# Kernel tuning notes

Measured on AMD Instinct MI355X. Metric: run time of the kernel, lower is better.

## Reference

```python
import jax, jax.numpy as jnp
import numpy as np

EPS = 1e-15
MAX_TANH_ARG = 1.0 - 1e-5  # clamp for artanh domain, standard in Poincare-ball libs


def logmap0(x):
    # Poincare ball, c=1: logmap0(x) = artanh(||x||) * x / ||x||
    norm = jnp.linalg.norm(x, axis=-1, keepdims=True)
    norm_c = jnp.clip(norm, EPS, MAX_TANH_ARG)
    scale = jnp.arctanh(norm_c) / jnp.maximum(norm, EPS)
    return scale * x


def expmap0(v):
    # Poincare ball, c=1: expmap0(v) = tanh(||v||) * v / ||v||
    norm = jnp.linalg.norm(v, axis=-1, keepdims=True)
    scale = jnp.tanh(norm) / jnp.maximum(norm, EPS)
    return scale * v


def setup_inputs() -> dict:
    key = jax.random.key(0)
    k1, k2, k3, k4 = jax.random.split(key, 4)
    N, E, D_IN, D_OUT = 50000, 600000, 128, 128
    # points loosely inside/near the ball; logmap0 clamps the norm anyway
    x = jax.random.uniform(k1, (N, D_IN), dtype=jnp.float32)
    edge_index = jax.random.randint(k2, (2, E), 0, N, dtype=jnp.int32)
    W = jax.random.normal(k3, (D_OUT, D_IN), dtype=jnp.float32) / np.sqrt(D_IN)
    b = jax.random.normal(k4, (D_OUT,), dtype=jnp.float32) * 0.01
    return {"x": x, "edge_index": edge_index, "W": W, "b": b}


def reference(x, edge_index, W, b):
    num_nodes = x.shape[0]
    src, dst = edge_index[0], edge_index[1]

    x_tangent = logmap0(x)                       # [N, D_in]
    h = x_tangent @ W.T + b                      # [N, D_out]

    # symmetric degree count: each edge adds 1 to dst and 1 to src
    ones = jnp.ones(src.shape[0], dtype=jnp.float32)
    deg = (jax.ops.segment_sum(ones, dst, num_segments=num_nodes)
           + jax.ops.segment_sum(ones, src, num_segments=num_nodes))
    deg = jnp.maximum(deg, 1.0)
    dinv = deg ** -0.5                           # [N]

    # fused gather-scale-scatter across ALL feature dims at once
    msg = h[src] * (dinv[src] * dinv[dst])[:, None]   # [E, D_out]
    out = jax.ops.segment_sum(msg, dst, num_segments=num_nodes)  # [N, D_out]

    return expmap0(out)
```

## Files before the change

### kernel.cpp

```cpp
#include <hip/hip_runtime.h>
#include <math.h>

#define D 128
#define CAP 48
#define NS 64
#define HB2 (NS * 2)
#define HBT (HB2 * 2)
#define HLDS 28672
#define BKB 128

typedef __attribute__((ext_vector_type(8))) short short8;
typedef __attribute__((ext_vector_type(4))) float f32x4;

__device__ inline unsigned short f2bf(float f) {
  unsigned int u = __float_as_uint(f);
  u = (u + 0x7FFFu + ((u >> 16) & 1u)) >> 16;
  return (unsigned short)u;
}
__device__ inline float bf2f(unsigned int us) {
  return __uint_as_float(us << 16);
}

__global__ __launch_bounds__(256) void k_prep(
    const float* __restrict__ W, const int* __restrict__ src,
    const int* __restrict__ dst, unsigned short* __restrict__ Wbf,
    unsigned int* __restrict__ cursor, unsigned char* __restrict__ part8,
    unsigned char* __restrict__ rank, int N, int E, int HP, int fancy) {
  const int t = threadIdx.x;
  const int bid = blockIdx.x;

  if (bid < HBT) {
    if (!fancy) return;
    __shared__ unsigned int lh[HLDS / 4];
    const int kind = bid >> 7;
    const int sb = bid & 127;
    const int s = sb >> 1, hf = sb & 1;
    const int H = (N + 1) >> 1;
    const int G16 = (H + 15) >> 4;
    for (int i = t; i < G16; i += 256) ((uint4*)lh)[i] = make_uint4(0, 0, 0, 0);
    __syncthreads();
    const int e0 = (int)((long long)s * E / NS);
    const int e1 = (int)((long long)(s + 1) * E / NS);
    const int hbase = hf * H;
    if (kind == 0) {
      for (int e = e0 + t; e < e1; e += 256) {
        int n = dst[e];
        unsigned int lw = (unsigned)(n - hbase);
        if (lw < (unsigned)H) {
          int sh = (lw & 3) << 3;
          unsigned int old = atomicAdd(&lh[lw >> 2], 1u << sh);
          rank[e] = (unsigned char)((old >> sh) & 0xFFu);
        }
      }
    } else {
      for (int e = e0 + t; e < e1; e += 256) {
        int n = src[e];
        unsigned int lw = (unsigned)(n - hbase);
        if (lw < (unsigned)H) atomicAdd(&lh[lw >> 2], 1u << ((lw & 3) << 3));
      }
    }
    __syncthreads();
    uint4* po = (uint4*)(part8 + (size_t)bid * HP);
    for (int i = t; i < G16; i += 256) po[i] = ((const uint4*)lh)[i];
    return;
  }

  int g = (bid - HBT) * 256 + t;
  if (g < N) cursor[g] = 0u;
  int i = g * 4;
  if (i < D * D) {
    float4 wv = *(const float4*)(W + i);
    int r = i >> 7, c = i & 127;
    int idx = ((c >> 3) << 10) + (r << 3) + (c & 7);
    *(ushort4*)(&Wbf[idx]) =
        make_ushort4(f2bf(wv.x), f2bf(wv.y), f2bf(wv.z), f2bf(wv.w));
  }
}

__global__ __launch_bounds__(256) void k_reduce(
    const unsigned char* __restrict__ part8, float* __restrict__ dinv,
    unsigned int* __restrict__ cntv, unsigned short* __restrict__ pre, int N,
    int HP) {
  int n = blockIdx.x * 256 + threadIdx.x;
  if (n >= N) return;
  const int H = (N + 1) >> 1;
  int hf = (n >= H);
  int lw = n - hf * H;
  unsigned int run = 0, so = 0;
  unsigned int pk[NS / 2];
#pragma unroll
  for (int s = 0; s < NS; ++s) {
    unsigned int cin = part8[(size_t)(s * 2 + hf) * HP + lw];
    unsigned int cot = part8[(size_t)(HB2 + s * 2 + hf) * HP + lw];
    if (s & 1)
      pk[s >> 1] |= run << 16;
    else
      pk[s >> 1] = run;
    run += cin;
    so += cot;
  }
  uint4* pp = (uint4*)(pre + (size_t)n * NS);
#pragma unroll
  for (int i = 0; i < NS / 8; ++i)
    pp[i] = make_uint4(pk[i * 4], pk[i * 4 + 1], pk[i * 4 + 2], pk[i * 4 + 3]);
  cntv[n] = run;
  dinv[n] = rsqrtf(fmaxf((float)(run + so), 1.0f));
}

__global__ __launch_bounds__(256) void k_main(
    const float* __restrict__ x, const unsigned short* __restrict__ Wbf,
    const float* __restrict__ bvec, const int* __restrict__ src,
    const int* __restrict__ dst, unsigned int* __restrict__ cursor,
    int* __restrict__ ebuf, const unsigned char* __restrict__ rank,
    const unsigned short* __restrict__ pre, unsigned short* __restrict__ h,
    int N, int E, int fancy) {
  const int t = threadIdx.x;
  const int bid = blockIdx.x;

  if (bid < BKB) {
    if (fancy) {
      const int s = bid >> 1;
      const int e0 = (int)((long long)s * E / NS);
      const int e1 = (int)((long long)(s + 1) * E / NS);
      for (int e = e0 + (bid & 1) * 256 + t; e < e1; e += 512) {
        int d_ = dst[e];
        unsigned int slot =
            (unsigned int)pre[(size_t)d_ * NS + s] + (unsigned int)rank[e];
        if (slot < CAP) ebuf[(size_t)d_ * CAP + slot] = src[e];
      }
    } else {
      const int e0 = (int)((long long)bid * E / BKB);
      const int e1 = (int)((long long)(bid + 1) * E / BKB);
      for (int e = e0 + t; e < e1; e += 256) {
        int d_ = dst[e], s_ = src[e];
        unsigned int p = atomicAdd(&cursor[d_], 1u) & 0xFFFFu;
        if (p < CAP) ebuf[(size_t)d_ * CAP + p] = s_;
        atomicAdd(&cursor[s_], 0x10000u);
      }
    }
    return;
  }

  const int gb = bid - BKB;
  const int w = t >> 6;
  const int l = t & 63;
  const int lc = l & 15;
  const int q = l >> 4;
  const int r0 = gb * 64;
  const int grow = r0 + w * 16 + lc;
  const bool ok = grow < N;
  const float* xp = x + (size_t)grow * D + q * 8;

  short8 a[4];
  float ss = 0.0f;
#pragma unroll
  for (int kk = 0; kk < 4; ++kk) {
    float4 u = ok ? *(const float4*)(xp + kk * 32) : make_float4(0, 0, 0, 0);
    float4 v = ok ? *(const float4*)(xp + kk * 32 + 4) : make_float4(0, 0, 0, 0);
    ss += u.x * u.x + u.y * u.y + u.z * u.z + u.w * u.w;
    ss += v.x * v.x + v.y * v.y + v.z * v.z + v.w * v.w;
    short8 af;
    af[0] = (short)f2bf(u.x); af[1] = (short)f2bf(u.y);
    af[2] = (short)f2bf(u.z); af[3] = (short)f2bf(u.w);
    af[4] = (short)f2bf(v.x); af[5] = (short)f2bf(v.y);
    af[6] = (short)f2bf(v.z); af[7] = (short)f2bf(v.w);
    a[kk] = af;
  }
  ss += __shfl_xor(ss, 16, 64);
  ss += __shfl_xor(ss, 32, 64);
  float nrm = sqrtf(ss);
  float nc = fminf(fmaxf(nrm, 1e-15f), 1.0f - 1e-5f);
  float rs = atanhf(nc) / fmaxf(nrm, 1e-15f);

  f32x4 acc[8];
#pragma unroll
  for (int nt = 0; nt < 8; ++nt) acc[nt] = (f32x4){0.f, 0.f, 0.f, 0.f};

#pragma unroll
  for (int kk = 0; kk < 4; ++kk) {
#pragma unroll
    for (int nt = 0; nt < 8; ++nt) {
      short8 bf =
          *(const short8*)(Wbf + ((kk * 4 + q) << 10) + ((nt * 16 + lc) << 3));
      acc[nt] = __builtin_amdgcn_mfma_f32_16x16x32_bf16(a[kk], bf, acc[nt], 0, 0, 0);
    }
  }

  float rsl[4];
#pragma unroll
  for (int i = 0; i < 4; ++i) rsl[i] = __shfl(rs, q * 4 + i, 64);

#pragma unroll
  for (int nt = 0; nt < 8; ++nt) {
    int j = nt * 16 + lc;
    float bj = bvec[j];
#pragma unroll
    for (int i = 0; i < 4; ++i) {
      int gr = r0 + w * 16 + q * 4 + i;
      if (gr < N) h[(size_t)gr * D + j] = f2bf(rsl[i] * acc[nt][i] + bj);
    }
  }
}

__global__ __launch_bounds__(256) void k_gather(
    const unsigned short* __restrict__ h, const int* __restrict__ ebuf,
    const unsigned int* __restrict__ cursor, const float* __restrict__ dinv,
    const unsigned int* __restrict__ cntv, float* __restrict__ out, int N,
    int fancy) {
  int gid = blockIdx.x * 256 + threadIdx.x;
  int r = gid >> 5;
  int sub = threadIdx.x & 31;
  if (r >= N) return;

  int cnt;
  float di_d;
  if (fancy) {
    cnt = (int)cntv[r];
    di_d = dinv[r];
  } else {
    unsigned int cr = cursor[r];
    cnt = (int)(cr & 0xFFFFu);
    di_d = rsqrtf(fmaxf((float)((cr & 0xFFFFu) + (cr >> 16)), 1.0f));
  }
  if (cnt > CAP) cnt = CAP;
  const int* eb = ebuf + (size_t)r * CAP;

  int c1 = cnt < 32 ? cnt : 32;
  int s_a = (sub < c1) ? eb[sub] : 0;
  float dv_a = 0.0f;
  if (sub < c1) {
    if (fancy) dv_a = dinv[s_a];
    else {
      unsigned int vs = cursor[s_a];
      dv_a = rsqrtf(fmaxf((float)((vs & 0xFFFFu) + (vs >> 16)), 1.0f));
    }
  }
  int s_b = (sub + 32 < cnt) ? eb[32 + sub] : 0;
  float dv_b = 0.0f;
  if (sub + 32 < cnt) {
    if (fancy) dv_b = dinv[s_b];
    else {
      unsigned int vs = cursor[s_b];
      dv_b = rsqrtf(fmaxf((float)((vs & 0xFFFFu) + (vs >> 16)), 1.0f));
    }
  }

  float a0 = 0.f, a1 = 0.f, a2 = 0.f, a3 = 0.f;
  for (int i = 0; i < c1; i += 8) {
    uint2 pv[8];
    float wj[8];
#pragma unroll
    for (int j = 0; j < 8; ++j) {
      int s = __shfl(s_a, i + j, 32);
      wj[j] = __shfl(dv_a, i + j, 32);
      pv[j] = *(const uint2*)(h + (size_t)s * D + sub * 4);
    }
#pragma unroll
    for (int j = 0; j < 8; ++j) {
      a0 += wj[j] * bf2f(pv[j].x & 0xFFFFu);
      a1 += wj[j] * bf2f(pv[j].x >> 16);
      a2 += wj[j] * bf2f(pv[j].y & 0xFFFFu);
      a3 += wj[j] * bf2f(pv[j].y >> 16);
    }
  }
  for (int i = 0; i < cnt - 32; i += 8) {
    uint2 pv[8];
    float wj[8];
#pragma unroll
    for (int j = 0; j < 8; ++j) {
      int s = __shfl(s_b, i + j, 32);
      wj[j] = __shfl(dv_b, i + j, 32);
      pv[j] = *(const uint2*)(h + (size_t)s * D + sub * 4);
    }
#pragma unroll
    for (int j = 0; j < 8; ++j) {
      a0 += wj[j] * bf2f(pv[j].x & 0xFFFFu);
      a1 += wj[j] * bf2f(pv[j].x >> 16);
      a2 += wj[j] * bf2f(pv[j].y & 0xFFFFu);
      a3 += wj[j] * bf2f(pv[j].y >> 16);
    }
  }

  a0 *= di_d; a1 *= di_d; a2 *= di_d; a3 *= di_d;

  float sN = a0 * a0 + a1 * a1 + a2 * a2 + a3 * a3;
#pragma unroll
  for (int off = 16; off > 0; off >>= 1) sN += __shfl_down(sN, off, 32);
  sN = __shfl(sN, 0, 32);
  float n = sqrtf(sN);
  float sc = tanhf(n) / fmaxf(n, 1e-15f);

  float4* op = (float4*)(out + (size_t)r * D);
  op[sub] = make_float4(a0 * sc, a1 * sc, a2 * sc, a3 * sc);
}

extern "C" void kernel_launch(void* const* d_in, const int* in_sizes, int n_in,
                              void* d_out, int out_size, void* d_ws, size_t ws_size,
                              hipStream_t stream) {
  const float* x = (const float*)d_in[0];
  const int* ei = (const int*)d_in[1];
  const float* W = (const float*)d_in[2];
  const float* b = (const float*)d_in[3];
  float* out = (float*)d_out;

  const int N = in_sizes[0] / D;
  const int E = in_sizes[1] / 2;
  const int* src = ei;
  const int* dst = ei + E;

  const int H = (N + 1) >> 1;
  const int HP = (H + 255) & ~255;

  size_t o_ebuf = ((size_t)N * D * 2 + 63) & ~(size_t)63;
  size_t o_cur = (o_ebuf + (size_t)N * CAP * 4 + 63) & ~(size_t)63;
  size_t o_dinv = (o_cur + (size_t)N * 4 + 63) & ~(size_t)63;
  size_t o_cnt = (o_dinv + (size_t)N * 4 + 63) & ~(size_t)63;
  size_t o_wbf = (o_cnt + (size_t)N * 4 + 63) & ~(size_t)63;
  size_t o_p8 = (o_wbf + 32768 + 255) & ~(size_t)255;
  size_t o_pre = (o_p8 + (size_t)HBT * HP + 63) & ~(size_t)63;
  size_t o_rank = (o_pre + (size_t)N * NS * 2 + 63) & ~(size_t)63;
  size_t need = o_rank + (size_t)E;

  unsigned short* h = (unsigned short*)d_ws;
  int* ebuf = (int*)((char*)d_ws + o_ebuf);
  unsigned int* cursor = (unsigned int*)((char*)d_ws + o_cur);
  float* dinv = (float*)((char*)d_ws + o_dinv);
  unsigned int* cntv = (unsigned int*)((char*)d_ws + o_cnt);
  unsigned short* Wbf = (unsigned short*)((char*)d_ws + o_wbf);
  unsigned char* part8 = (unsigned char*)((char*)d_ws + o_p8);
  unsigned short* pre = (unsigned short*)((char*)d_ws + o_pre);
  unsigned char* rank = (unsigned char*)((char*)d_ws + o_rank);

  const int fancy = (H <= HLDS) && (N <= 65535) && (ws_size >= need);

  int PBn = (N + 255) / 256;
  int PB = PBn > 16 ? PBn : 16;
  k_prep<<<HBT + PB, 256, 0, stream>>>(W, src, dst, Wbf, cursor, part8, rank, N,
                                       E, HP, fancy);

  if (fancy)
    k_reduce<<<(N + 255) / 256, 256, 0, stream>>>(part8, dinv, cntv, pre, N, HP);

  const int NBG = (N + 63) / 64;
  k_main<<<BKB + NBG, 256, 0, stream>>>(x, Wbf, b, src, dst, cursor, ebuf, rank,
                                        pre, h, N, E, fancy);
  k_gather<<<(int)(((long long)N * 32 + 255) / 256), 256, 0, stream>>>(
      h, ebuf, cursor, dinv, cntv, out, N, fancy);
}
```

Before: 148.8 us.

## Use full-range LDS histograms with 1024-thread blocks and slice-major prefix layout

The degree/rank histogram blocks now cover all N nodes in a 56KB LDS histogram instead of splitting nodes into two halves. Each block runs 1024 threads, and there are 128 edge slices instead of 64. Prefix offsets are stored slice-major as packed 32-bit pairs, so k_reduce writes coalesced and the bucketing pass reads one contiguous array per slice. Each edge is now read once per histogram rather than twice with half filtered out. The trade-offs are higher LDS use per block, which lowers occupancy, and more partial histograms for k_reduce to sum.

```diff
diff --git a/kernel.cpp b/kernel.cpp
--- a/kernel.cpp
+++ b/kernel.cpp
@@ -3,10 +3,9 @@
 
 #define D 128
 #define CAP 48
-#define NS 64
-#define HB2 (NS * 2)
-#define HBT (HB2 * 2)
-#define HLDS 28672
+#define NS 128
+#define HBT (NS * 2)
+#define HLDSB 57344
 #define BKB 128
 
 typedef __attribute__((ext_vector_type(8))) short short8;
@@ -21,7 +20,7 @@
   return __uint_as_float(us << 16);
 }
 
-__global__ __launch_bounds__(256) void k_prep(
+__global__ __launch_bounds__(1024) void k_prep(
     const float* __restrict__ W, const int* __restrict__ src,
     const int* __restrict__ dst, unsigned short* __restrict__ Wbf,
     unsigned int* __restrict__ cursor, unsigned char* __restrict__ part8,
@@ -31,41 +30,34 @@
 
   if (bid < HBT) {
     if (!fancy) return;
-    __shared__ unsigned int lh[HLDS / 4];
+    __shared__ unsigned int lh[HLDSB / 4];
     const int kind = bid >> 7;
-    const int sb = bid & 127;
-    const int s = sb >> 1, hf = sb & 1;
-    const int H = (N + 1) >> 1;
-    const int G16 = (H + 15) >> 4;
-    for (int i = t; i < G16; i += 256) ((uint4*)lh)[i] = make_uint4(0, 0, 0, 0);
+    const int s = bid & (NS - 1);
+    const int G16 = (N + 15) >> 4;
+    for (int i = t; i < G16; i += 1024) ((uint4*)lh)[i] = make_uint4(0, 0, 0, 0);
     __syncthreads();
     const int e0 = (int)((long long)s * E / NS);
     const int e1 = (int)((long long)(s + 1) * E / NS);
-    const int hbase = hf * H;
     if (kind == 0) {
-      for (int e = e0 + t; e < e1; e += 256) {
-        int n = dst[e];
-        unsigned int lw = (unsigned)(n - hbase);
-        if (lw < (unsigned)H) {
-          int sh = (lw & 3) << 3;
-          unsigned int old = atomicAdd(&lh[lw >> 2], 1u << sh);
-          rank[e] = (unsigned char)((old >> sh) & 0xFFu);
-        }
+      for (int e = e0 + t; e < e1; e += 1024) {
+        unsigned int n = (unsigned)dst[e];
+        int sh = (n & 3) << 3;
+        unsigned int old = atomicAdd(&lh[n >> 2], 1u << sh);
+        rank[e] = (unsigned char)((old >> sh) & 0xFFu);
       }
     } else {
-      for (int e = e0 + t; e < e1; e += 256) {
-        int n = src[e];
-        unsigned int lw = (unsigned)(n - hbase);
-        if (lw < (unsigned)H) atomicAdd(&lh[lw >> 2], 1u << ((lw & 3) << 3));
+      for (int e = e0 + t; e < e1; e += 1024) {
+        unsigned int n = (unsigned)src[e];
+        atomicAdd(&lh[n >> 2], 1u << ((n & 3) << 3));
       }
     }
     __syncthreads();
     uint4* po = (uint4*)(part8 + (size_t)bid * HP);
-    for (int i = t; i < G16; i += 256) po[i] = ((const uint4*)lh)[i];
+    for (int i = t; i < G16; i += 1024) po[i] = ((const uint4*)lh)[i];
     return;
   }
 
-  int g = (bid - HBT) * 256 + t;
+  int g = (bid - HBT) * 1024 + t;
   if (g < N) cursor[g] = 0u;
   int i = g * 4;
   if (i < D * D) {
@@ -79,30 +71,24 @@
 
 __global__ __launch_bounds__(256) void k_reduce(
     const unsigned char* __restrict__ part8, float* __restrict__ dinv,
-    unsigned int* __restrict__ cntv, unsigned short* __restrict__ pre, int N,
+    unsigned int* __restrict__ cntv, unsigned int* __restrict__ pre32, int N,
     int HP) {
   int n = blockIdx.x * 256 + threadIdx.x;
   if (n >= N) return;
-  const int H = (N + 1) >> 1;
-  int hf = (n >= H);
-  int lw = n - hf * H;
   unsigned int run = 0, so = 0;
-  unsigned int pk[NS / 2];
-#pragma unroll
-  for (int s = 0; s < NS; ++s) {
-    unsigned int cin = part8[(size_t)(s * 2 + hf) * HP + lw];
-    unsigned int cot = part8[(size_t)(HB2 + s * 2 + hf) * HP + lw];
-    if (s & 1)
-      pk[s >> 1] |= run << 16;
-    else
-      pk[s >> 1] = run;
-    run += cin;
-    so += cot;
-  }
-  uint4* pp = (uint4*)(pre + (size_t)n * NS);
-#pragma unroll
-  for (int i = 0; i < NS / 8; ++i)
-    pp[i] = make_uint4(pk[i * 4], pk[i * 4 + 1], pk[i * 4 + 2], pk[i * 4 + 3]);
+#pragma unroll 8
+  for (int g = 0; g < NS / 2; ++g) {
+    unsigned int c0 = part8[(size_t)(2 * g) * HP + n];
+    unsigned int c1 = part8[(size_t)(2 * g + 1) * HP + n];
+    unsigned int o0 = part8[(size_t)(NS + 2 * g) * HP + n];
+    unsigned int o1 = part8[(size_t)(NS + 2 * g + 1) * HP + n];
+    unsigned int w = run & 0xFFFFu;
+    run += c0;
+    w |= (run & 0xFFFFu) << 16;
+    run += c1;
+    so += o0 + o1;
+    pre32[(size_t)g * N + n] = w;
+  }
   cntv[n] = run;
   dinv[n] = rsqrtf(fmaxf((float)(run + so), 1.0f));
 }
@@ -112,20 +98,21 @@
     const float* __restrict__ bvec, const int* __restrict__ src,
     const int* __restrict__ dst, unsigned int* __restrict__ cursor,
     int* __restrict__ ebuf, const unsigned char* __restrict__ rank,
-    const unsigned short* __restrict__ pre, unsigned short* __restrict__ h,
+    const unsigned int* __restrict__ pre32, unsigned short* __restrict__ h,
     int N, int E, int fancy) {
   const int t = threadIdx.x;
   const int bid = blockIdx.x;
 
   if (bid < BKB) {
     if (fancy) {
-      const int s = bid >> 1;
+      const int s = bid;
       const int e0 = (int)((long long)s * E / NS);
       const int e1 = (int)((long long)(s + 1) * E / NS);
-      for (int e = e0 + (bid & 1) * 256 + t; e < e1; e += 512) {
+      const unsigned int* ps = pre32 + (size_t)(s >> 1) * N;
+      const int sh = (s & 1) << 4;
+      for (int e = e0 + t; e < e1; e += 256) {
         int d_ = dst[e];
-        unsigned int slot =
-            (unsigned int)pre[(size_t)d_ * NS + s] + (unsigned int)rank[e];
+        unsigned int slot = ((ps[d_] >> sh) & 0xFFFFu) + (unsigned int)rank[e];
         if (slot < CAP) ebuf[(size_t)d_ * CAP + slot] = src[e];
       }
     } else {
@@ -308,8 +295,7 @@
   const int* src = ei;
   const int* dst = ei + E;
 
-  const int H = (N + 1) >> 1;
-  const int HP = (H + 255) & ~255;
+  const int HP = (N + 255) & ~255;
 
   size_t o_ebuf = ((size_t)N * D * 2 + 63) & ~(size_t)63;
   size_t o_cur = (o_ebuf + (size_t)N * CAP * 4 + 63) & ~(size_t)63;
@@ -318,7 +304,7 @@
   size_t o_wbf = (o_cnt + (size_t)N * 4 + 63) & ~(size_t)63;
   size_t o_p8 = (o_wbf + 32768 + 255) & ~(size_t)255;
   size_t o_pre = (o_p8 + (size_t)HBT * HP + 63) & ~(size_t)63;
-  size_t o_rank = (o_pre + (size_t)N * NS * 2 + 63) & ~(size_t)63;
+  size_t o_rank = (o_pre + (size_t)(NS / 2) * N * 4 + 63) & ~(size_t)63;
   size_t need = o_rank + (size_t)E;
 
   unsigned short* h = (unsigned short*)d_ws;
@@ -328,22 +314,23 @@
   unsigned int* cntv = (unsigned int*)((char*)d_ws + o_cnt);
   unsigned short* Wbf = (unsigned short*)((char*)d_ws + o_wbf);
   unsigned char* part8 = (unsigned char*)((char*)d_ws + o_p8);
-  unsigned short* pre = (unsigned short*)((char*)d_ws + o_pre);
+  unsigned int* pre32 = (unsigned int*)((char*)d_ws + o_pre);
   unsigned char* rank = (unsigned char*)((char*)d_ws + o_rank);
 
-  const int fancy = (H <= HLDS) && (N <= 65535) && (ws_size >= need);
-
-  int PBn = (N + 255) / 256;
-  int PB = PBn > 16 ? PBn : 16;
-  k_prep<<<HBT + PB, 256, 0, stream>>>(W, src, dst, Wbf, cursor, part8, rank, N,
-                                       E, HP, fancy);
+  const int fancy = (N <= HLDSB) && (N <= 65535) && (ws_size >= need);
+
+  int PB = (N + 1023) / 1024;
+  if (PB < 4) PB = 4;
+  k_prep<<<HBT + PB, 1024, 0, stream>>>(W, src, dst, Wbf, cursor, part8, rank,
+                                        N, E, HP, fancy);
 
   if (fancy)
-    k_reduce<<<(N + 255) / 256, 256, 0, stream>>>(part8, dinv, cntv, pre, N, HP);
+    k_reduce<<<(N + 255) / 256, 256, 0, stream>>>(part8, dinv, cntv, pre32, N,
+                                                  HP);
 
   const int NBG = (N + 63) / 64;
   k_main<<<BKB + NBG, 256, 0, stream>>>(x, Wbf, b, src, dst, cursor, ebuf, rank,
-                                        pre, h, N, E, fancy);
+                                        pre32, h, N, E, fancy);
   k_gather<<<(int)(((long long)N * 32 + 255) / 256), 256, 0, stream>>>(
       h, ebuf, cursor, dinv, cntv, out, N, fancy);
 }
```

Measured after the change: 141.2 us. 1.05x faster.
